# Performance work log

Measured on AMD Instinct MI355X. Metric: run time of the kernel, lower is better.

The kernel has to match this reference:

```python
import jax, jax.numpy as jnp
import numpy as np

EMBED_DIM = 768
NUM_HEAD = 12
HEAD_DIM = EMBED_DIM // NUM_HEAD


def setup_inputs() -> dict:
    key = jax.random.key(0)
    ks = jax.random.split(key, 9)
    B, S, E = 1, 4096, EMBED_DIM
    s = 1.0 / np.sqrt(E)
    inp = {
        "x": jax.random.normal(ks[0], (B, S, E), dtype=jnp.float32),
        "mask": jnp.zeros((B, S), dtype=jnp.bool_),  # True = masked out (padding)
        "Wq": jax.random.normal(ks[1], (E, E), dtype=jnp.float32) * s,
        "bq": jnp.zeros((E,), dtype=jnp.float32),
        "Wk": jax.random.normal(ks[2], (E, E), dtype=jnp.float32) * s,
        "bk": jnp.zeros((E,), dtype=jnp.float32),
        "Wv": jax.random.normal(ks[3], (E, E), dtype=jnp.float32) * s,
        "bv": jnp.zeros((E,), dtype=jnp.float32),
        "Wo": jax.random.normal(ks[4], (E, E), dtype=jnp.float32) * s,
        "bo": jnp.zeros((E,), dtype=jnp.float32),
    }
    return inp


def reference(x, mask, Wq, bq, Wk, bk, Wv, bv, Wo, bo):
    B, S, E = x.shape
    H, D = NUM_HEAD, HEAD_DIM
    # QKV projections -> [B, H, S, D]
    q = (x @ Wq.T + bq).reshape(B, S, H, D).transpose(0, 2, 1, 3)
    k = (x @ Wk.T + bk).reshape(B, S, H, D).transpose(0, 2, 1, 3)
    v = (x @ Wv.T + bv).reshape(B, S, H, D).transpose(0, 2, 1, 3)
    # NOTE: original scales by sqrt(embed_dim), not sqrt(head_dim)
    attn = jnp.einsum("bhqd,bhkd->bhqk", q, k) / jnp.sqrt(jnp.float32(E))
    # mask: [B, S] -> broadcast over (head, query) dims; True -> -inf
    attn = jnp.where(mask[:, None, None, :], -jnp.inf, attn)
    attn = jax.nn.softmax(attn, axis=-1)  # same math as manual max-subtract softmax
    out = jnp.einsum("bhqk,bhkd->bhqd", attn, v)  # [B, H, S, D]
    out = out.transpose(0, 2, 1, 3).reshape(B, S, E)
    return out @ Wo.T + bo
```

## Files before the change

kernel.cpp:

```cpp
#include <hip/hip_runtime.h>
#include <hip/hip_bf16.h>
#include <math.h>

typedef __bf16 bf16;
typedef __attribute__((ext_vector_type(8))) __bf16 bf16x8;
typedef __attribute__((ext_vector_type(4))) __bf16 bf16x4;
typedef __attribute__((ext_vector_type(4))) float f32x4;

typedef __attribute__((address_space(1))) void* as1ptr;
typedef __attribute__((address_space(3))) void* as3ptr;

__device__ __forceinline__ void gload16(const void* g, void* lds) {
  __builtin_amdgcn_global_load_lds((as1ptr)(unsigned long long)(g),
                                   (as3ptr)(unsigned long long)(lds), 16, 0, 0);
}

#define MFMA16(a, b, c) __builtin_amdgcn_mfma_f32_16x16x32_bf16((a), (b), (c), 0, 0, 0)
#define EXP2(x) __builtin_amdgcn_exp2f(x)
#define WAITV4 asm volatile("s_waitcnt vmcnt(4)" ::: "memory")
#define WAITV0 asm volatile("s_waitcnt vmcnt(0)" ::: "memory")
#define BAR() __builtin_amdgcn_s_barrier()
#define PRIO1() __builtin_amdgcn_s_setprio(1)
#define PRIO0() __builtin_amdgcn_s_setprio(0)

#define SEQ 4096
#define EMB 768
#define QSC (0.036084391824351615f * 1.4426950408889634f)

#define NCVT 2688
__global__ __launch_bounds__(256)
void cvt_all_kernel(const float* __restrict__ x, const float* __restrict__ Wq,
                    const float* __restrict__ Wk, const float* __restrict__ Wv,
                    const float* __restrict__ Wo,
                    bf16* __restrict__ xb, bf16* __restrict__ Wqb, bf16* __restrict__ Wkb,
                    bf16* __restrict__ Wvb, bf16* __restrict__ Wob,
                    const unsigned char* __restrict__ mask,
                    unsigned long long* __restrict__ tf64) {
  int b = blockIdx.x;
  if (b == NCVT) {
    int t = threadIdx.x;
    if (t < 64) {
      unsigned v = 0;
      const unsigned char* mp = mask + t * 64;
      for (int i = 0; i < 64; i++) v |= mp[i];
      unsigned long long bits = __ballot(v != 0);
      if (t == 0) *tf64 = bits;
    }
    return;
  }
  const float* in;
  bf16* out;
  int base;
  if (b < 1536) {
    in = x; out = xb; base = b;
  } else {
    int r = b - 1536, seg = r / 288, off = r % 288;
    in  = (seg == 0) ? Wq  : (seg == 1) ? Wk  : (seg == 2) ? Wv  : Wo;
    out = (seg == 0) ? Wqb : (seg == 1) ? Wkb : (seg == 2) ? Wvb : Wob;
    base = off;
  }
  int i = (base * 256 + threadIdx.x) * 8;
  float4 a = *(const float4*)(in + i);
  float4 c = *(const float4*)(in + i + 4);
  bf16x8 v;
  v[0] = (bf16)a.x; v[1] = (bf16)a.y; v[2] = (bf16)a.z; v[3] = (bf16)a.w;
  v[4] = (bf16)c.x; v[5] = (bf16)c.y; v[6] = (bf16)c.z; v[7] = (bf16)c.w;
  *(bf16x8*)(out + i) = v;
}

template <int MODE>
__global__ __launch_bounds__(256)
void gemm_bt_kernel(const bf16* __restrict__ A,
                    const bf16* __restrict__ B0, const bf16* __restrict__ B1,
                    const bf16* __restrict__ B2,
                    const float* __restrict__ bias0, const float* __restrict__ bias1,
                    const float* __restrict__ bias2,
                    float* __restrict__ outF, bf16* __restrict__ Qh,
                    char* __restrict__ Kswz, char* __restrict__ Vswz) {
  __shared__ __attribute__((aligned(16))) char Asb[3][8192];
  __shared__ __attribute__((aligned(16))) char Bsb[3][8192];
  const int tid = threadIdx.x;
  const int wid = tid >> 6, lane = tid & 63;
  const int g = lane >> 4, c16 = lane & 15;
  const int wr = wid >> 1, wc = wid & 1;
  const int bm0 = blockIdx.x * 128;

  const bf16* Bp;
  const float* bias;
  int nb, mat = 0;
  if (MODE == 1) {
    mat = blockIdx.y / 6;
    nb = (blockIdx.y % 6) * 128;
    Bp = (mat == 0) ? B0 : (mat == 1 ? B1 : B2);
    bias = (mat == 0) ? bias0 : (mat == 1 ? bias1 : bias2);
  } else {
    nb = blockIdx.y * 128;
    Bp = B0;
    bias = bias0;
  }

  const int arow = tid >> 2, acol = (tid & 3) * 16;

#define STAGE_G(k, b)                                                              \
  do {                                                                             \
    gload16((const char*)A + (size_t)(bm0 + arow) * (EMB * 2) + (k)*64 + acol,     \
            &Asb[b][wid * 1024]);                                                  \
    gload16((const char*)A + (size_t)(bm0 + 64 + arow) * (EMB * 2) + (k)*64 + acol,\
            &Asb[b][4096 + wid * 1024]);                                           \
    gload16((const char*)Bp + (size_t)(nb + arow) * (EMB * 2) + (k)*64 + acol,     \
            &Bsb[b][wid * 1024]);                                                  \
    gload16((const char*)Bp + (size_t)(nb + 64 + arow) * (EMB * 2) + (k)*64 + acol,\
            &Bsb[b][4096 + wid * 1024]);                                           \
  } while (0)

  f32x4 acc[4][4];
#pragma unroll
  for (int i = 0; i < 4; i++)
#pragma unroll
    for (int j = 0; j < 4; j++) acc[i][j] = f32x4{0.f, 0.f, 0.f, 0.f};

#define COMPUTE_G(cur)                                                         \
  do {                                                                         \
    bf16x8 a[4], b[4];                                                         \
    _Pragma("unroll") for (int i = 0; i < 4; i++)                              \
        a[i] = *(const bf16x8*)(&Asb[cur][(wr * 64 + i * 16 + c16) * 64 + g * 16]); \
    _Pragma("unroll") for (int j = 0; j < 4; j++)                              \
        b[j] = *(const bf16x8*)(&Bsb[cur][(wc * 64 + j * 16 + c16) * 64 + g * 16]); \
    PRIO1();                                                                   \
    _Pragma("unroll") for (int i = 0; i < 4; i++)                              \
        _Pragma("unroll") for (int j = 0; j < 4; j++)                          \
            acc[i][j] = MFMA16(a[i], b[j], acc[i][j]);                         \
    PRIO0();                                                                   \
  } while (0)

  STAGE_G(0, 0);
  STAGE_G(1, 1);
  int cur = 0;
  for (int kk = 0; kk < EMB / 32 - 1; ++kk) {
    WAITV4;
    BAR();
    if (kk < EMB / 32 - 2) {
      int stb = (cur == 0) ? 2 : cur - 1;
      STAGE_G(kk + 2, stb);
    }
    COMPUTE_G(cur);
    cur = (cur == 2) ? 0 : cur + 1;
  }
  WAITV0;
  BAR();
  COMPUTE_G(cur);
#undef STAGE_G
#undef COMPUTE_G

#pragma unroll
  for (int i = 0; i < 4; i++) {
#pragma unroll
    for (int j = 0; j < 4; j++) {
      int colL = nb + wc * 64 + j * 16 + c16;
      float bval = bias[colL];
#pragma unroll
      for (int r = 0; r < 4; r++) {
        int row = bm0 + wr * 64 + i * 16 + 4 * g + r;
        float val = acc[i][j][r] + bval;
        if (MODE == 0) {
          outF[(size_t)row * EMB + colL] = val;
        } else {
          int hh = colL >> 6, d = colL & 63;
          if (mat == 0) {
            Qh[((size_t)hh * SEQ + row) * 64 + d] = (bf16)(val * QSC);
          } else if (mat == 1) {
            *(bf16*)(Kswz + ((size_t)hh * SEQ + row) * 128 +
                     ((d * 2) ^ ((row & 7) << 4))) = (bf16)val;
          } else {
            int u5 = 8 * ((row & 15) >> 2) + 4 * ((row >> 4) & 1) + (row & 3);
            int cc = (row & 32) | u5;
            *(bf16*)(Vswz + ((size_t)hh * 64 + d) * 8192 + (size_t)(row >> 6) * 128 +
                     ((cc * 2) ^ ((d & 7) << 4))) = (bf16)val;
          }
        }
      }
    }
  }
}

__global__ __launch_bounds__(256)
void attn_kernel(const char* __restrict__ Kswz, const char* __restrict__ Vswz,
                 const bf16* __restrict__ Qh, const unsigned char* __restrict__ mask,
                 const unsigned long long* __restrict__ tf64, bf16* __restrict__ O) {
  __shared__ __attribute__((aligned(16))) char Kt[3][8192];
  __shared__ __attribute__((aligned(16))) char Vt[3][8192];
  const int tid = threadIdx.x;
  const int wid = tid >> 6, lane = tid & 63;
  const int g = (lane >> 4) & 3, c16 = lane & 15;
  const int h = blockIdx.y;
  const int q0 = blockIdx.x * 64 + wid * 16;
  const unsigned long long tfb = *tf64;

  bf16x8 qa0, qa1;
  {
    const bf16* qp = Qh + ((size_t)h * SEQ + q0 + c16) * 64 + g * 8;
    qa0 = *(const bf16x8*)(qp);
    qa1 = *(const bf16x8*)(qp + 32);
  }

  f32x4 ot[4];
#pragma unroll
  for (int f = 0; f < 4; ++f) ot[f] = f32x4{0.f, 0.f, 0.f, 0.f};
  float m_ = -1e38f, l_ = 0.f;

  const char* ksrc = Kswz + (size_t)h * SEQ * 128 + tid * 16;
  const char* vsrc0 = Vswz + ((size_t)h * 64 + (tid >> 3)) * 8192 + (tid & 7) * 16;
  const char* vsrc1 = Vswz + ((size_t)h * 64 + 32 + (tid >> 3)) * 8192 + (tid & 7) * 16;

#define STAGE(t, b)                                                    \
  do {                                                                 \
    gload16(ksrc + (size_t)(t)*8192,        &Kt[b][wid * 1024]);       \
    gload16(ksrc + (size_t)(t)*8192 + 4096, &Kt[b][4096 + wid * 1024]);\
    gload16(vsrc0 + (size_t)(t)*128, &Vt[b][wid * 1024]);              \
    gload16(vsrc1 + (size_t)(t)*128, &Vt[b][4096 + wid * 1024]);       \
  } while (0)

#define COMPUTE(t, cur)                                                         \
  do {                                                                          \
    const char* Kb = Kt[cur];                                                   \
    const char* Vb = Vt[cur];                                                   \
    f32x4 sc[4];                                                                \
    bf16x8 k0[4], k1[4];                                                        \
    _Pragma("unroll") for (int cf = 0; cf < 4; ++cf) {                          \
      int row = cf * 16 + c16, sw = (row & 7) << 4;                             \
      k0[cf] = *(const bf16x8*)(Kb + row * 128 + ((g * 16) ^ sw));              \
      k1[cf] = *(const bf16x8*)(Kb + row * 128 + ((64 + g * 16) ^ sw));         \
    }                                                                           \
    PRIO1();                                                                    \
    _Pragma("unroll") for (int cf = 0; cf < 4; ++cf) {                          \
      f32x4 z = f32x4{0.f, 0.f, 0.f, 0.f};                                      \
      z = MFMA16(k0[cf], qa0, z);                                               \
      z = MFMA16(k1[cf], qa1, z);                                               \
      sc[cf] = z;                                                               \
    }                                                                           \
    PRIO0();                                                                    \
    if (tfb & (1ull << (t))) {                                                  \
      _Pragma("unroll") for (int cf = 0; cf < 4; ++cf)                          \
          _Pragma("unroll") for (int r = 0; r < 4; r++)                         \
              if (mask[(t)*64 + cf * 16 + 4 * g + r]) sc[cf][r] = -INFINITY;    \
    }                                                                           \
    float x0 = fmaxf(fmaxf(sc[0][0], sc[0][1]), fmaxf(sc[0][2], sc[0][3]));     \
    float x1 = fmaxf(fmaxf(sc[1][0], sc[1][1]), fmaxf(sc[1][2], sc[1][3]));     \
    float x2 = fmaxf(fmaxf(sc[2][0], sc[2][1]), fmaxf(sc[2][2], sc[2][3]));     \
    float x3 = fmaxf(fmaxf(sc[3][0], sc[3][1]), fmaxf(sc[3][2], sc[3][3]));     \
    float mt = fmaxf(fmaxf(x0, x1), fmaxf(x2, x3));                             \
    mt = fmaxf(mt, __shfl_xor(mt, 16));                                         \
    mt = fmaxf(mt, __shfl_xor(mt, 32));                                         \
    if (__any(mt > m_ + 8.f)) {                                                 \
      float mn = fmaxf(m_, mt);                                                 \
      float corr = EXP2(m_ - mn);                                               \
      l_ *= corr;                                                               \
      _Pragma("unroll") for (int f = 0; f < 4; ++f) ot[f] *= corr;              \
      m_ = mn;                                                                  \
    }                                                                           \
    float p[16];                                                                \
    _Pragma("unroll") for (int cf = 0; cf < 4; ++cf)                            \
        _Pragma("unroll") for (int r = 0; r < 4; r++)                           \
            p[cf * 4 + r] = EXP2(sc[cf][r] - m_);                               \
    l_ += ((p[0] + p[1]) + (p[2] + p[3])) + ((p[4] + p[5]) + (p[6] + p[7])) +   \
          (((p[8] + p[9]) + (p[10] + p[11])) + ((p[12] + p[13]) + (p[14] + p[15]))); \
    bf16x8 pb0, pb1;                                                            \
    _Pragma("unroll") for (int e = 0; e < 8; ++e) {                             \
      pb0[e] = (bf16)p[e];                                                      \
      pb1[e] = (bf16)p[8 + e];                                                  \
    }                                                                           \
    bf16x8 v0[4], v1[4];                                                        \
    _Pragma("unroll") for (int f = 0; f < 4; ++f) {                             \
      int row = f * 16 + c16, sw = (row & 7) << 4;                              \
      v0[f] = *(const bf16x8*)(Vb + row * 128 + ((g * 16) ^ sw));               \
      v1[f] = *(const bf16x8*)(Vb + row * 128 + ((64 + g * 16) ^ sw));          \
    }                                                                           \
    PRIO1();                                                                    \
    _Pragma("unroll") for (int f = 0; f < 4; ++f) {                             \
      ot[f] = MFMA16(v0[f], pb0, ot[f]);                                        \
      ot[f] = MFMA16(v1[f], pb1, ot[f]);                                        \
    }                                                                           \
    PRIO0();                                                                    \
  } while (0)

  STAGE(0, 0);
  STAGE(1, 1);
  int cur = 0;
  for (int t = 0; t < SEQ / 64 - 1; ++t) {
    WAITV4;
    BAR();
    if (t < SEQ / 64 - 2) {
      int stb = (cur == 0) ? 2 : cur - 1;
      STAGE(t + 2, stb);
    }
    COMPUTE(t, cur);
    cur = (cur == 2) ? 0 : cur + 1;
  }
  WAITV0;
  BAR();
  COMPUTE(SEQ / 64 - 1, cur);
#undef STAGE
#undef COMPUTE

  l_ += __shfl_xor(l_, 16);
  l_ += __shfl_xor(l_, 32);
  float inv = 1.f / l_;
#pragma unroll
  for (int f = 0; f < 4; ++f) {
    bf16x4 w;
#pragma unroll
    for (int r = 0; r < 4; r++) w[r] = (bf16)(ot[f][r] * inv);
    *(bf16x4*)(O + (size_t)(q0 + c16) * EMB + h * 64 + f * 16 + 4 * g) = w;
  }
}

extern "C" void kernel_launch(void* const* d_in, const int* in_sizes, int n_in,
                              void* d_out, int out_size, void* d_ws, size_t ws_size,
                              hipStream_t stream) {
  (void)in_sizes; (void)n_in; (void)out_size; (void)ws_size;
  const float* x = (const float*)d_in[0];
  const unsigned char* mask = (const unsigned char*)d_in[1];
  const float* Wq = (const float*)d_in[2];
  const float* bq = (const float*)d_in[3];
  const float* Wk = (const float*)d_in[4];
  const float* bk = (const float*)d_in[5];
  const float* Wv = (const float*)d_in[6];
  const float* bv = (const float*)d_in[7];
  const float* Wo = (const float*)d_in[8];
  const float* bo = (const float*)d_in[9];
  float* out = (float*)d_out;
  char* ws = (char*)d_ws;

  bf16* xb   = (bf16*)(ws + 0);
  bf16* Wqb  = (bf16*)(ws + 6291456);
  bf16* Wkb  = (bf16*)(ws + 7471104);
  bf16* Wvb  = (bf16*)(ws + 8650752);
  bf16* Wob  = (bf16*)(ws + 9830400);
  bf16* Qh   = (bf16*)(ws + 11010048);
  char* Kswz = ws + 17301504;
  char* Vswz = ws + 23592960;
  bf16* Obuf = (bf16*)(ws + 29884416);
  unsigned long long* tf64 = (unsigned long long*)(ws + 36175872);

  cvt_all_kernel<<<NCVT + 1, 256, 0, stream>>>(x, Wq, Wk, Wv, Wo, xb, Wqb, Wkb, Wvb,
                                               Wob, mask, tf64);
  gemm_bt_kernel<1><<<dim3(32, 18), 256, 0, stream>>>(
      xb, Wqb, Wkb, Wvb, bq, bk, bv, nullptr, Qh, Kswz, Vswz);
  attn_kernel<<<dim3(64, 12), 256, 0, stream>>>(Kswz, Vswz, Qh, mask, tf64, Obuf);
  gemm_bt_kernel<0><<<dim3(32, 6), 256, 0, stream>>>(
      Obuf, Wob, nullptr, nullptr, bo, nullptr, nullptr, out, nullptr, nullptr, nullptr);
}
```

Before: 144.2 us.

## Switch attention to 32x32 MFMA with split-KV waves and merge partials

The attention kernel now uses 32x32x16 bf16 MFMA instead of 16x16x32. Each wave handles 32 queries and half of each 64-key tile, so waves are split two ways over queries and two ways over keys. The V swizzle layout in the projection epilogue changes to match the new operand layout. At the end, per-wave softmax max and sum are exchanged through LDS and the two key-half partial outputs are merged before writing. This is meant to cut LDS fragment reads and MFMA issue count per tile, at the cost of an extra cross-wave reduction in the epilogue and more accumulator registers.

```diff
diff --git a/kernel.cpp b/kernel.cpp
--- a/kernel.cpp
+++ b/kernel.cpp
@@ -6,6 +6,7 @@
 typedef __attribute__((ext_vector_type(8))) __bf16 bf16x8;
 typedef __attribute__((ext_vector_type(4))) __bf16 bf16x4;
 typedef __attribute__((ext_vector_type(4))) float f32x4;
+typedef __attribute__((ext_vector_type(16))) float f32x16;
 
 typedef __attribute__((address_space(1))) void* as1ptr;
 typedef __attribute__((address_space(3))) void* as3ptr;
@@ -16,6 +17,7 @@
 }
 
 #define MFMA16(a, b, c) __builtin_amdgcn_mfma_f32_16x16x32_bf16((a), (b), (c), 0, 0, 0)
+#define MFMA32(a, b, c) __builtin_amdgcn_mfma_f32_32x32x16_bf16((a), (b), (c), 0, 0, 0)
 #define EXP2(x) __builtin_amdgcn_exp2f(x)
 #define WAITV4 asm volatile("s_waitcnt vmcnt(4)" ::: "memory")
 #define WAITV0 asm volatile("s_waitcnt vmcnt(0)" ::: "memory")
@@ -172,8 +174,8 @@
             *(bf16*)(Kswz + ((size_t)hh * SEQ + row) * 128 +
                      ((d * 2) ^ ((row & 7) << 4))) = (bf16)val;
           } else {
-            int u5 = 8 * ((row & 15) >> 2) + 4 * ((row >> 4) & 1) + (row & 3);
-            int cc = (row & 32) | u5;
+            int kk2 = row & 63;
+            int cc = (kk2 & 48) | (kk2 & 3) | ((kk2 & 4) << 1) | ((kk2 & 8) >> 1);
             *(bf16*)(Vswz + ((size_t)hh * 64 + d) * 8192 + (size_t)(row >> 6) * 128 +
                      ((cc * 2) ^ ((d & 7) << 4))) = (bf16)val;
           }
@@ -191,21 +193,24 @@
   __shared__ __attribute__((aligned(16))) char Vt[3][8192];
   const int tid = threadIdx.x;
   const int wid = tid >> 6, lane = tid & 63;
-  const int g = (lane >> 4) & 3, c16 = lane & 15;
+  const int qh = wid >> 1, kh = wid & 1;
+  const int l31 = lane & 31, hi = lane >> 5;
   const int h = blockIdx.y;
-  const int q0 = blockIdx.x * 64 + wid * 16;
+  const int q0 = blockIdx.x * 64;
   const unsigned long long tfb = *tf64;
 
-  bf16x8 qa0, qa1;
+  bf16x8 qa[4];
   {
-    const bf16* qp = Qh + ((size_t)h * SEQ + q0 + c16) * 64 + g * 8;
-    qa0 = *(const bf16x8*)(qp);
-    qa1 = *(const bf16x8*)(qp + 32);
-  }
-
-  f32x4 ot[4];
-#pragma unroll
-  for (int f = 0; f < 4; ++f) ot[f] = f32x4{0.f, 0.f, 0.f, 0.f};
+    const bf16* qp = Qh + ((size_t)h * SEQ + q0 + qh * 32 + l31) * 64 + hi * 8;
+    qa[0] = *(const bf16x8*)(qp);
+    qa[1] = *(const bf16x8*)(qp + 16);
+    qa[2] = *(const bf16x8*)(qp + 32);
+    qa[3] = *(const bf16x8*)(qp + 48);
+  }
+
+  f32x16 ot0, ot1;
+#pragma unroll
+  for (int r = 0; r < 16; r++) { ot0[r] = 0.f; ot1[r] = 0.f; }
   float m_ = -1e38f, l_ = 0.f;
 
   const char* ksrc = Kswz + (size_t)h * SEQ * 128 + tid * 16;
@@ -220,67 +225,68 @@
     gload16(vsrc1 + (size_t)(t)*128, &Vt[b][4096 + wid * 1024]);       \
   } while (0)
 
-#define COMPUTE(t, cur)                                                         \
-  do {                                                                          \
-    const char* Kb = Kt[cur];                                                   \
-    const char* Vb = Vt[cur];                                                   \
-    f32x4 sc[4];                                                                \
-    bf16x8 k0[4], k1[4];                                                        \
-    _Pragma("unroll") for (int cf = 0; cf < 4; ++cf) {                          \
-      int row = cf * 16 + c16, sw = (row & 7) << 4;                             \
-      k0[cf] = *(const bf16x8*)(Kb + row * 128 + ((g * 16) ^ sw));              \
-      k1[cf] = *(const bf16x8*)(Kb + row * 128 + ((64 + g * 16) ^ sw));         \
-    }                                                                           \
-    PRIO1();                                                                    \
-    _Pragma("unroll") for (int cf = 0; cf < 4; ++cf) {                          \
-      f32x4 z = f32x4{0.f, 0.f, 0.f, 0.f};                                      \
-      z = MFMA16(k0[cf], qa0, z);                                               \
-      z = MFMA16(k1[cf], qa1, z);                                               \
-      sc[cf] = z;                                                               \
-    }                                                                           \
-    PRIO0();                                                                    \
-    if (tfb & (1ull << (t))) {                                                  \
-      _Pragma("unroll") for (int cf = 0; cf < 4; ++cf)                          \
-          _Pragma("unroll") for (int r = 0; r < 4; r++)                         \
-              if (mask[(t)*64 + cf * 16 + 4 * g + r]) sc[cf][r] = -INFINITY;    \
-    }                                                                           \
-    float x0 = fmaxf(fmaxf(sc[0][0], sc[0][1]), fmaxf(sc[0][2], sc[0][3]));     \
-    float x1 = fmaxf(fmaxf(sc[1][0], sc[1][1]), fmaxf(sc[1][2], sc[1][3]));     \
-    float x2 = fmaxf(fmaxf(sc[2][0], sc[2][1]), fmaxf(sc[2][2], sc[2][3]));     \
-    float x3 = fmaxf(fmaxf(sc[3][0], sc[3][1]), fmaxf(sc[3][2], sc[3][3]));     \
-    float mt = fmaxf(fmaxf(x0, x1), fmaxf(x2, x3));                             \
-    mt = fmaxf(mt, __shfl_xor(mt, 16));                                         \
-    mt = fmaxf(mt, __shfl_xor(mt, 32));                                         \
-    if (__any(mt > m_ + 8.f)) {                                                 \
-      float mn = fmaxf(m_, mt);                                                 \
-      float corr = EXP2(m_ - mn);                                               \
-      l_ *= corr;                                                               \
-      _Pragma("unroll") for (int f = 0; f < 4; ++f) ot[f] *= corr;              \
-      m_ = mn;                                                                  \
-    }                                                                           \
-    float p[16];                                                                \
-    _Pragma("unroll") for (int cf = 0; cf < 4; ++cf)                            \
-        _Pragma("unroll") for (int r = 0; r < 4; r++)                           \
-            p[cf * 4 + r] = EXP2(sc[cf][r] - m_);                               \
-    l_ += ((p[0] + p[1]) + (p[2] + p[3])) + ((p[4] + p[5]) + (p[6] + p[7])) +   \
-          (((p[8] + p[9]) + (p[10] + p[11])) + ((p[12] + p[13]) + (p[14] + p[15]))); \
-    bf16x8 pb0, pb1;                                                            \
-    _Pragma("unroll") for (int e = 0; e < 8; ++e) {                             \
-      pb0[e] = (bf16)p[e];                                                      \
-      pb1[e] = (bf16)p[8 + e];                                                  \
-    }                                                                           \
-    bf16x8 v0[4], v1[4];                                                        \
-    _Pragma("unroll") for (int f = 0; f < 4; ++f) {                             \
-      int row = f * 16 + c16, sw = (row & 7) << 4;                              \
-      v0[f] = *(const bf16x8*)(Vb + row * 128 + ((g * 16) ^ sw));               \
-      v1[f] = *(const bf16x8*)(Vb + row * 128 + ((64 + g * 16) ^ sw));          \
-    }                                                                           \
-    PRIO1();                                                                    \
-    _Pragma("unroll") for (int f = 0; f < 4; ++f) {                             \
-      ot[f] = MFMA16(v0[f], pb0, ot[f]);                                        \
-      ot[f] = MFMA16(v1[f], pb1, ot[f]);                                        \
-    }                                                                           \
-    PRIO0();                                                                    \
+  const int krow = kh * 32 + l31;
+  const int ksw = (krow & 7) << 4;
+  const int vsw = (l31 & 7) << 4;
+  const int vcb = kh * 64 + hi * 16;
+
+#define COMPUTE(t, cur)                                                          \
+  do {                                                                           \
+    const char* Kb = Kt[cur];                                                    \
+    const char* Vb = Vt[cur];                                                    \
+    bf16x8 kf0 = *(const bf16x8*)(Kb + krow * 128 + ((hi * 16) ^ ksw));          \
+    bf16x8 kf1 = *(const bf16x8*)(Kb + krow * 128 + ((32 + hi * 16) ^ ksw));     \
+    bf16x8 kf2 = *(const bf16x8*)(Kb + krow * 128 + ((64 + hi * 16) ^ ksw));     \
+    bf16x8 kf3 = *(const bf16x8*)(Kb + krow * 128 + ((96 + hi * 16) ^ ksw));     \
+    f32x16 s;                                                                    \
+    _Pragma("unroll") for (int r = 0; r < 16; r++) s[r] = 0.f;                   \
+    PRIO1();                                                                     \
+    s = MFMA32(kf0, qa[0], s);                                                   \
+    s = MFMA32(kf1, qa[1], s);                                                   \
+    s = MFMA32(kf2, qa[2], s);                                                   \
+    s = MFMA32(kf3, qa[3], s);                                                   \
+    PRIO0();                                                                     \
+    if (tfb & (1ull << (t))) {                                                   \
+      _Pragma("unroll") for (int r = 0; r < 16; r++) {                           \
+        int key = (t)*64 + kh * 32 + (r & 3) + 8 * (r >> 2) + 4 * hi;            \
+        if (mask[key]) s[r] = -INFINITY;                                         \
+      }                                                                          \
+    }                                                                            \
+    float m01 = fmaxf(fmaxf(s[0], s[1]), fmaxf(s[2], s[3]));                     \
+    float m23 = fmaxf(fmaxf(s[4], s[5]), fmaxf(s[6], s[7]));                     \
+    float m45 = fmaxf(fmaxf(s[8], s[9]), fmaxf(s[10], s[11]));                   \
+    float m67 = fmaxf(fmaxf(s[12], s[13]), fmaxf(s[14], s[15]));                 \
+    float mt = fmaxf(fmaxf(m01, m23), fmaxf(m45, m67));                          \
+    mt = fmaxf(mt, __shfl_xor(mt, 32));                                          \
+    if (__any(mt > m_ + 8.f)) {                                                  \
+      float mn = fmaxf(m_, mt);                                                  \
+      float corr = EXP2(m_ - mn);                                                \
+      l_ *= corr;                                                                \
+      ot0 *= corr;                                                               \
+      ot1 *= corr;                                                               \
+      m_ = mn;                                                                   \
+    }                                                                            \
+    float p[16];                                                                 \
+    _Pragma("unroll") for (int r = 0; r < 16; r++) p[r] = EXP2(s[r] - m_);       \
+    float ls = (((p[0] + p[1]) + (p[2] + p[3])) + ((p[4] + p[5]) + (p[6] + p[7]))) + \
+               (((p[8] + p[9]) + (p[10] + p[11])) + ((p[12] + p[13]) + (p[14] + p[15]))); \
+    ls += __shfl_xor(ls, 32);                                                    \
+    l_ += ls;                                                                    \
+    bf16x8 pb0, pb1;                                                             \
+    _Pragma("unroll") for (int e = 0; e < 8; ++e) {                              \
+      pb0[e] = (bf16)p[e];                                                       \
+      pb1[e] = (bf16)p[8 + e];                                                   \
+    }                                                                            \
+    bf16x8 vf00 = *(const bf16x8*)(Vb + l31 * 128 + ((vcb) ^ vsw));              \
+    bf16x8 vf01 = *(const bf16x8*)(Vb + l31 * 128 + ((vcb + 32) ^ vsw));         \
+    bf16x8 vf10 = *(const bf16x8*)(Vb + (32 + l31) * 128 + ((vcb) ^ vsw));       \
+    bf16x8 vf11 = *(const bf16x8*)(Vb + (32 + l31) * 128 + ((vcb + 32) ^ vsw));  \
+    PRIO1();                                                                     \
+    ot0 = MFMA32(vf00, pb0, ot0);                                                \
+    ot0 = MFMA32(vf01, pb1, ot0);                                                \
+    ot1 = MFMA32(vf10, pb0, ot1);                                                \
+    ot1 = MFMA32(vf11, pb1, ot1);                                                \
+    PRIO0();                                                                     \
   } while (0)
 
   STAGE(0, 0);
@@ -302,15 +308,49 @@
 #undef STAGE
 #undef COMPUTE
 
-  l_ += __shfl_xor(l_, 16);
-  l_ += __shfl_xor(l_, 32);
-  float inv = 1.f / l_;
-#pragma unroll
-  for (int f = 0; f < 4; ++f) {
-    bf16x4 w;
-#pragma unroll
-    for (int r = 0; r < 4; r++) w[r] = (bf16)(ot[f][r] * inv);
-    *(bf16x4*)(O + (size_t)(q0 + c16) * EMB + h * 64 + f * 16 + 4 * g) = w;
+  __syncthreads();
+  float* ml = (float*)&Vt[0][0];
+  ml[(wid * 64 + lane) * 2 + 0] = m_;
+  ml[(wid * 64 + lane) * 2 + 1] = l_;
+  __syncthreads();
+  const int pw = wid ^ 1;
+  float m2 = ml[(pw * 64 + lane) * 2 + 0];
+  float l2 = ml[(pw * 64 + lane) * 2 + 1];
+  float M = fmaxf(m_, m2);
+  float al = EXP2(m_ - M);
+  float lt = al * l_ + EXP2(m2 - M) * l2;
+  ot0 *= al;
+  ot1 *= al;
+  char* ob = (char*)&Kt[0][0];
+  char* obase = ob + qh * 8192 + lane * 128;
+  const int osw = (lane & 7) << 4;
+  if (kh == 1) {
+#pragma unroll
+    for (int u = 0; u < 4; ++u) {
+      f32x4 w0 = {ot0[4 * u], ot0[4 * u + 1], ot0[4 * u + 2], ot0[4 * u + 3]};
+      f32x4 w1 = {ot1[4 * u], ot1[4 * u + 1], ot1[4 * u + 2], ot1[4 * u + 3]};
+      *(f32x4*)(obase + ((u * 16) ^ osw)) = w0;
+      *(f32x4*)(obase + (((4 + u) * 16) ^ osw)) = w1;
+    }
+  }
+  __syncthreads();
+  if (kh == 0) {
+    float inv = 1.f / lt;
+    int tok = q0 + qh * 32 + l31;
+    bf16* op = O + (size_t)tok * EMB + h * 64;
+#pragma unroll
+    for (int u = 0; u < 4; ++u) {
+      f32x4 w0 = *(const f32x4*)(obase + ((u * 16) ^ osw));
+      f32x4 w1 = *(const f32x4*)(obase + (((4 + u) * 16) ^ osw));
+      bf16x4 o0, o1;
+#pragma unroll
+      for (int e = 0; e < 4; ++e) {
+        o0[e] = (bf16)((ot0[4 * u + e] + w0[e]) * inv);
+        o1[e] = (bf16)((ot1[4 * u + e] + w1[e]) * inv);
+      }
+      *(bf16x4*)(op + 8 * u + 4 * hi) = o0;
+      *(bf16x4*)(op + 32 + 8 * u + 4 * hi) = o1;
+    }
   }
 }
 
```

Result: no change. 144.6 us (+0.3%).
